# Optimization experiments

Hardware: AMD Instinct MI355X
Metric: run time of the kernel (lower is better)

The kernel has to match this reference:

```python
import jax, jax.numpy as jnp
import numpy as np

B, T, D = 32, 2048, 1024


def setup_inputs() -> dict:
    key = jax.random.key(0)
    k1, k2, k3, k4, k5, k6 = jax.random.split(key, 6)
    return {
        "keys": jax.random.normal(k1, (B, T, D), dtype=jnp.float32),
        "value": jax.random.normal(k2, (B, T, D), dtype=jnp.float32),
        "query": jax.random.normal(k3, (B, D), dtype=jnp.float32),
        "weight_feedback": jax.random.normal(k4, (B, T, D), dtype=jnp.float32),
        "v": jax.random.normal(k5, (D,), dtype=jnp.float32) / np.sqrt(D),
        "enc_seq_len": jax.random.randint(k6, (B,), 1, T + 1, dtype=jnp.int32),
    }


def reference(keys, value, query, weight_feedback, v, enc_seq_len):
    # energies = v^T tanh(key + query + weight_feedback)  -> [B, T]
    hidden = jnp.tanh(keys + query[:, None, :] + weight_feedback)  # [B,T,D]
    energies = jnp.einsum("btd,d->bt", hidden, v)                  # [B,T]
    # length mask + softmax over time
    mask = jnp.arange(energies.shape[1])[None, :] < enc_seq_len[:, None]  # [B,T]
    energies = jnp.where(mask, energies, -jnp.inf)
    weights = jax.nn.softmax(energies, axis=1)                      # [B,T]
    # context = weights^T value -> [B, D_v]
    context = jnp.einsum("bt,btd->bd", weights, value)
    return context, weights[:, :, None]
```

## Files before the change

kernel.cpp:

```cpp
#include <hip/hip_runtime.h>
#include <math.h>

#define BB 32
#define TT 2048
#define DD 1024
#define TCHUNK 64

__device__ __forceinline__ float fast_tanh(float x) {
    float e = __expf(2.0f * x);
    return 1.0f - __fdividef(2.0f, e + 1.0f);
}

__global__ __launch_bounds__(256) void energies_kernel(
    const float* __restrict__ keys, const float* __restrict__ query,
    const float* __restrict__ wf, const float* __restrict__ v,
    const int* __restrict__ lenp, float* __restrict__ eout)
{
    const int t = blockIdx.x;
    const int b = blockIdx.y;
    if (t >= lenp[b]) return;

    const int d = threadIdx.x * 4;
    const size_t row = ((size_t)b * TT + t) * DD;

    const float4 k4 = *(const float4*)(keys + row + d);
    const float4 w4 = *(const float4*)(wf   + row + d);
    const float4 q4 = *(const float4*)(query + (size_t)b * DD + d);
    const float4 v4 = *(const float4*)(v + d);

    float s = fast_tanh(k4.x + q4.x + w4.x) * v4.x
            + fast_tanh(k4.y + q4.y + w4.y) * v4.y
            + fast_tanh(k4.z + q4.z + w4.z) * v4.z
            + fast_tanh(k4.w + q4.w + w4.w) * v4.w;

    #pragma unroll
    for (int off = 32; off > 0; off >>= 1) s += __shfl_down(s, off, 64);
    __shared__ float red[4];
    if ((threadIdx.x & 63) == 0) red[threadIdx.x >> 6] = s;
    __syncthreads();
    if (threadIdx.x == 0)
        eout[(size_t)b * TT + t] = red[0] + red[1] + red[2] + red[3];
}

__global__ __launch_bounds__(256) void softmax_kernel(
    const int* __restrict__ lenp, float* __restrict__ wrow_all)
{
    const int b = blockIdx.x;
    const int L = lenp[b];
    float* wrow = wrow_all + (size_t)b * TT;

    float e[8];
    float m = -INFINITY;
    #pragma unroll
    for (int i = 0; i < 8; i++) {
        const int t = threadIdx.x + i * 256;
        e[i] = (t < L) ? wrow[t] : -INFINITY;
        m = fmaxf(m, e[i]);
    }
    #pragma unroll
    for (int off = 1; off < 64; off <<= 1) m = fmaxf(m, __shfl_xor(m, off, 64));
    __shared__ float redm[4];
    const int wv = threadIdx.x >> 6;
    if ((threadIdx.x & 63) == 0) redm[wv] = m;
    __syncthreads();
    m = fmaxf(fmaxf(redm[0], redm[1]), fmaxf(redm[2], redm[3]));

    float s = 0.0f;
    #pragma unroll
    for (int i = 0; i < 8; i++) {
        e[i] = (e[i] == -INFINITY) ? 0.0f : __expf(e[i] - m);
        s += e[i];
    }
    #pragma unroll
    for (int off = 1; off < 64; off <<= 1) s += __shfl_xor(s, off, 64);
    __shared__ float reds[4];
    if ((threadIdx.x & 63) == 0) reds[wv] = s;
    __syncthreads();
    s = reds[0] + reds[1] + reds[2] + reds[3];
    const float inv = 1.0f / s;

    #pragma unroll
    for (int i = 0; i < 8; i++)
        wrow[threadIdx.x + i * 256] = e[i] * inv;
}

__global__ __launch_bounds__(256) void context_kernel(
    const float* __restrict__ value, const float* __restrict__ weights,
    const int* __restrict__ lenp, float* __restrict__ context)
{
    const int b = blockIdx.y;
    const int L = lenp[b];
    const int t0 = blockIdx.x * TCHUNK;
    if (t0 >= L) return;
    const int tend = min(t0 + TCHUNK, L);
    const int d = threadIdx.x * 4;

    float4 acc = make_float4(0.f, 0.f, 0.f, 0.f);
    for (int t = t0; t < tend; t++) {
        const float w = weights[(size_t)b * TT + t];
        const float4 v4 = *(const float4*)(value + ((size_t)b * TT + t) * DD + d);
        acc.x += w * v4.x; acc.y += w * v4.y;
        acc.z += w * v4.z; acc.w += w * v4.w;
    }
    float* dst = context + (size_t)b * DD + d;
    atomicAdd(dst + 0, acc.x);
    atomicAdd(dst + 1, acc.y);
    atomicAdd(dst + 2, acc.z);
    atomicAdd(dst + 3, acc.w);
}

extern "C" void kernel_launch(void* const* d_in, const int* in_sizes, int n_in,
                              void* d_out, int out_size, void* d_ws, size_t ws_size,
                              hipStream_t stream) {
    const float* keys  = (const float*)d_in[0];
    const float* value = (const float*)d_in[1];
    const float* query = (const float*)d_in[2];
    const float* wf    = (const float*)d_in[3];
    const float* v     = (const float*)d_in[4];
    const int*   lenp  = (const int*)d_in[5];

    float* out      = (float*)d_out;
    float* context  = out;
    float* weights  = out + BB * DD;

    hipMemsetAsync(context, 0, (size_t)BB * DD * sizeof(float), stream);

    energies_kernel<<<dim3(TT, BB), 256, 0, stream>>>(keys, query, wf, v, lenp, weights);
    softmax_kernel<<<BB, 256, 0, stream>>>(lenp, weights);
    context_kernel<<<dim3(TT / TCHUNK, BB), 256, 0, stream>>>(value, weights, lenp, context);
}
```

Baseline: 599.0 us.

## Process multiple rows per wave in energies; replace atomics with partial-sum reduction

The energies kernel now gives each wavefront 8 time rows, and each block handles 32 rows. Query and v are loaded once per wave and reused across those rows, and the cross-wave shared-memory reduction is dropped. This cuts launch count and per-row block overhead. The context step now writes per-chunk partial sums to workspace, and a second kernel reduces them, replacing the memset and atomicAdds when the workspace is large enough; this adds an extra kernel launch and some workspace traffic.

Result: slower. 613.6 us (+2.4%).

```diff
diff --git a/kernel.cpp b/kernel.cpp
--- a/kernel.cpp
+++ b/kernel.cpp
@@ -4,7 +4,11 @@
 #define BB 32
 #define TT 2048
 #define DD 1024
-#define TCHUNK 64
+
+#define EROWS_PER_WAVE  8
+#define EROWS_PER_BLOCK 32
+#define CCHUNK 64
+#define NCHUNK (TT / CCHUNK)
 
 __device__ __forceinline__ float fast_tanh(float x) {
     float e = __expf(2.0f * x);
@@ -16,30 +20,45 @@
     const float* __restrict__ wf, const float* __restrict__ v,
     const int* __restrict__ lenp, float* __restrict__ eout)
 {
-    const int t = blockIdx.x;
     const int b = blockIdx.y;
-    if (t >= lenp[b]) return;
-
-    const int d = threadIdx.x * 4;
-    const size_t row = ((size_t)b * TT + t) * DD;
-
-    const float4 k4 = *(const float4*)(keys + row + d);
-    const float4 w4 = *(const float4*)(wf   + row + d);
-    const float4 q4 = *(const float4*)(query + (size_t)b * DD + d);
-    const float4 v4 = *(const float4*)(v + d);
-
-    float s = fast_tanh(k4.x + q4.x + w4.x) * v4.x
-            + fast_tanh(k4.y + q4.y + w4.y) * v4.y
-            + fast_tanh(k4.z + q4.z + w4.z) * v4.z
-            + fast_tanh(k4.w + q4.w + w4.w) * v4.w;
-
-    #pragma unroll
-    for (int off = 32; off > 0; off >>= 1) s += __shfl_down(s, off, 64);
-    __shared__ float red[4];
-    if ((threadIdx.x & 63) == 0) red[threadIdx.x >> 6] = s;
-    __syncthreads();
-    if (threadIdx.x == 0)
-        eout[(size_t)b * TT + t] = red[0] + red[1] + red[2] + red[3];
+    const int L = lenp[b];
+    const int t0 = blockIdx.x * EROWS_PER_BLOCK;
+    if (t0 >= L) return;
+
+    const int lane = threadIdx.x & 63;
+    const int wv   = threadIdx.x >> 6;
+    const int d0   = lane * 4;
+
+    float4 q[4], vv[4];
+    #pragma unroll
+    for (int j = 0; j < 4; j++) {
+        q[j]  = *(const float4*)(query + (size_t)b * DD + j * 256 + d0);
+        vv[j] = *(const float4*)(v + j * 256 + d0);
+    }
+
+    const int tBeg = t0 + wv * EROWS_PER_WAVE;
+    const int tEnd = min(tBeg + EROWS_PER_WAVE, L);
+    for (int t = tBeg; t < tEnd; t++) {
+        const size_t row = ((size_t)b * TT + t) * DD;
+        float4 k[4], w[4];
+        #pragma unroll
+        for (int j = 0; j < 4; j++) {
+            k[j] = *(const float4*)(keys + row + j * 256 + d0);
+            w[j] = *(const float4*)(wf   + row + j * 256 + d0);
+        }
+        float s = 0.0f;
+        #pragma unroll
+        for (int j = 0; j < 4; j++) {
+            s += vv[j].x * fast_tanh(k[j].x + q[j].x + w[j].x);
+            s += vv[j].y * fast_tanh(k[j].y + q[j].y + w[j].y);
+            s += vv[j].z * fast_tanh(k[j].z + q[j].z + w[j].z);
+            s += vv[j].w * fast_tanh(k[j].w + q[j].w + w[j].w);
+        }
+        #pragma unroll
+        for (int off = 32; off > 0; off >>= 1)
+            s += __shfl_xor(s, off, 64);
+        if (lane == 0) eout[(size_t)b * TT + t] = s;
+    }
 }
 
 __global__ __launch_bounds__(256) void softmax_kernel(
@@ -84,15 +103,60 @@
         wrow[threadIdx.x + i * 256] = e[i] * inv;
 }
 
-__global__ __launch_bounds__(256) void context_kernel(
+__global__ __launch_bounds__(256) void context_partial_kernel(
+    const float* __restrict__ value, const float* __restrict__ weights,
+    const int* __restrict__ lenp, float* __restrict__ partial)
+{
+    const int b = blockIdx.y;
+    const int L = lenp[b];
+    const int c = blockIdx.x;
+    const int t0 = c * CCHUNK;
+    if (t0 >= L) return;
+    const int tend = min(t0 + CCHUNK, L);
+    const int d = threadIdx.x * 4;
+
+    __shared__ float wsh[CCHUNK];
+    if (threadIdx.x < CCHUNK) {
+        const int t = t0 + threadIdx.x;
+        wsh[threadIdx.x] = (t < L) ? weights[(size_t)b * TT + t] : 0.0f;
+    }
+    __syncthreads();
+
+    float4 acc = make_float4(0.f, 0.f, 0.f, 0.f);
+    #pragma unroll 4
+    for (int t = t0; t < tend; t++) {
+        const float wt = wsh[t - t0];
+        const float4 v4 = *(const float4*)(value + ((size_t)b * TT + t) * DD + d);
+        acc.x += wt * v4.x; acc.y += wt * v4.y;
+        acc.z += wt * v4.z; acc.w += wt * v4.w;
+    }
+    *(float4*)(partial + ((size_t)c * BB + b) * DD + d) = acc;
+}
+
+__global__ __launch_bounds__(256) void context_reduce_kernel(
+    const float* __restrict__ partial, const int* __restrict__ lenp,
+    float* __restrict__ context)
+{
+    const int b = blockIdx.x;
+    const int nch = (lenp[b] + CCHUNK - 1) / CCHUNK;
+    const int d = threadIdx.x * 4;
+    float4 acc = make_float4(0.f, 0.f, 0.f, 0.f);
+    for (int c = 0; c < nch; c++) {
+        const float4 p = *(const float4*)(partial + ((size_t)c * BB + b) * DD + d);
+        acc.x += p.x; acc.y += p.y; acc.z += p.z; acc.w += p.w;
+    }
+    *(float4*)(context + (size_t)b * DD + d) = acc;
+}
+
+__global__ __launch_bounds__(256) void context_atomic_kernel(
     const float* __restrict__ value, const float* __restrict__ weights,
     const int* __restrict__ lenp, float* __restrict__ context)
 {
     const int b = blockIdx.y;
     const int L = lenp[b];
-    const int t0 = blockIdx.x * TCHUNK;
+    const int t0 = blockIdx.x * CCHUNK;
     if (t0 >= L) return;
-    const int tend = min(t0 + TCHUNK, L);
+    const int tend = min(t0 + CCHUNK, L);
     const int d = threadIdx.x * 4;
 
     float4 acc = make_float4(0.f, 0.f, 0.f, 0.f);
@@ -123,9 +187,19 @@
     float* context  = out;
     float* weights  = out + BB * DD;
 
-    hipMemsetAsync(context, 0, (size_t)BB * DD * sizeof(float), stream);
-
-    energies_kernel<<<dim3(TT, BB), 256, 0, stream>>>(keys, query, wf, v, lenp, weights);
+    energies_kernel<<<dim3(TT / EROWS_PER_BLOCK, BB), 256, 0, stream>>>(
+        keys, query, wf, v, lenp, weights);
     softmax_kernel<<<BB, 256, 0, stream>>>(lenp, weights);
-    context_kernel<<<dim3(TT / TCHUNK, BB), 256, 0, stream>>>(value, weights, lenp, context);
-}
+
+    const size_t need = (size_t)NCHUNK * BB * DD * sizeof(float);
+    if (d_ws != nullptr && ws_size >= need) {
+        float* partial = (float*)d_ws;
+        context_partial_kernel<<<dim3(NCHUNK, BB), 256, 0, stream>>>(
+            value, weights, lenp, partial);
+        context_reduce_kernel<<<BB, 256, 0, stream>>>(partial, lenp, context);
+    } else {
+        hipMemsetAsync(context, 0, (size_t)BB * DD * sizeof(float), stream);
+        context_atomic_kernel<<<dim3(NCHUNK, BB), 256, 0, stream>>>(
+            value, weights, lenp, context);
+    }
+}
```
